# Optimization experiments

Hardware: AMD Instinct MI355X
Metric: run time of the kernel (lower is better)

Reference implementation:

```python
import jax, jax.numpy as jnp
import numpy as np

N_SRC, N_DST, E = 10000, 40000, 1_280_000
IN_DIM, OUT_DIM, FEAT, O_DIM = 128, 64, 64, 300


def setup_inputs() -> dict:
    key = jax.random.key(0)
    ks = jax.random.split(key, 10)
    s = 0.05
    return {
        "h": jax.random.normal(ks[0], (N_SRC, IN_DIM), jnp.float32),
        "o": jax.random.normal(ks[1], (N_DST, O_DIM), jnp.float32),
        "tfidf": jax.random.normal(ks[2], (E, FEAT), jnp.float32),
        "W_fc": jax.random.normal(ks[3], (IN_DIM, OUT_DIM), jnp.float32) * s,
        "W_fc1": jax.random.normal(ks[4], (O_DIM, OUT_DIM), jnp.float32) * s,
        "W_feat": jax.random.normal(ks[5], (FEAT, OUT_DIM), jnp.float32) * s,
        "b_feat": jax.random.normal(ks[6], (OUT_DIM,), jnp.float32) * s,
        "W_attn": jax.random.normal(ks[7], (OUT_DIM, 1), jnp.float32) * s,
        "edge_src": jax.random.randint(ks[8], (E,), 0, N_SRC, jnp.int32),
        "edge_dst": jax.random.randint(ks[9], (E,), 0, N_DST, jnp.int32),
    }


def reference(h, o, tfidf, W_fc, W_fc1, W_feat, b_feat, W_attn, edge_src, edge_dst):
    n_dst = o.shape[0]
    # node projections: z on sentence (src) nodes via fc, on word (dst) nodes via fc1
    z_src = h @ W_fc                      # [N_SRC, D]
    z_dst = o @ W_fc1                     # [N_DST, D]
    # edge attention: z2 = src.z + dst.z + feat_fc(tfidfembed)
    dfeat = tfidf @ W_feat + b_feat       # [E, D]
    z2 = z_src[edge_src] + z_dst[edge_dst] + dfeat
    z3 = jnp.where(z2 > 0, z2, 0.01 * z2)  # leaky_relu, torch default slope
    e = (z3 @ W_attn)[:, 0]               # [E]
    # segment softmax over incoming edges of each dst (word) node
    m = jax.ops.segment_max(e, edge_dst, num_segments=n_dst)   # [N_DST]
    e_exp = jnp.exp(e - m[edge_dst])                           # [E]
    denom = jax.ops.segment_sum(e_exp, edge_dst, num_segments=n_dst)
    alpha = e_exp / jnp.maximum(denom, 1e-9)[edge_dst]         # [E]
    # weighted sum of src z into dst mailbox
    out = jax.ops.segment_sum(alpha[:, None] * z_src[edge_src], edge_dst,
                              num_segments=n_dst)              # [N_DST, D]
    return out
```

## Files before the change

kernel.cpp:

```cpp
#include <hip/hip_runtime.h>
#include <hip/hip_bf16.h>

#define N_SRC 10000
#define N_DST 40000
#define NE    1280000
#define IN_DIM 128
#define O_DIM  300
#define D      64
#define FEAT   64
#define NB     157

typedef __bf16 bf16x8 __attribute__((ext_vector_type(8)));
typedef __bf16 bf16x4 __attribute__((ext_vector_type(4)));
typedef float  f32x4  __attribute__((ext_vector_type(4)));

__global__ __launch_bounds__(256) void k_zsrc(const float* __restrict__ h,
                                              const float* __restrict__ Wfc,
                                              float* __restrict__ z,
                                              __bf16* __restrict__ zh){
    __shared__ float w[IN_DIM * D];
    for (int i = threadIdx.x; i < IN_DIM * D; i += blockDim.x) w[i] = Wfc[i];
    __syncthreads();
    int lane = threadIdx.x & 63;
    int wid  = blockIdx.x * 4 + (threadIdx.x >> 6);
    int nw   = gridDim.x * 4;
    for (int r0 = wid * 4; r0 < N_SRC; r0 += nw * 4){
        const f32x4* p0 = (const f32x4*)(h + (size_t)(r0 + 0) * IN_DIM);
        const f32x4* p1 = (const f32x4*)(h + (size_t)(r0 + 1) * IN_DIM);
        const f32x4* p2 = (const f32x4*)(h + (size_t)(r0 + 2) * IN_DIM);
        const f32x4* p3 = (const f32x4*)(h + (size_t)(r0 + 3) * IN_DIM);
        float a0 = 0.f, a1 = 0.f, a2 = 0.f, a3 = 0.f;
        #pragma unroll 4
        for (int k4 = 0; k4 < IN_DIM / 4; ++k4){
            f32x4 v0 = p0[k4], v1 = p1[k4], v2 = p2[k4], v3 = p3[k4];
            #pragma unroll
            for (int i = 0; i < 4; ++i){
                float wv = w[(k4 * 4 + i) * D + lane];
                a0 += v0[i] * wv; a1 += v1[i] * wv;
                a2 += v2[i] * wv; a3 += v3[i] * wv;
            }
        }
        z[(size_t)(r0 + 0) * D + lane] = a0; zh[(size_t)(r0 + 0) * D + lane] = (__bf16)a0;
        z[(size_t)(r0 + 1) * D + lane] = a1; zh[(size_t)(r0 + 1) * D + lane] = (__bf16)a1;
        z[(size_t)(r0 + 2) * D + lane] = a2; zh[(size_t)(r0 + 2) * D + lane] = (__bf16)a2;
        z[(size_t)(r0 + 3) * D + lane] = a3; zh[(size_t)(r0 + 3) * D + lane] = (__bf16)a3;
    }
}

__global__ __launch_bounds__(256) void k_zdst(const float* __restrict__ o,
                                              const float* __restrict__ Wfc1,
                                              float* __restrict__ z){
    extern __shared__ float w[];
    for (int i = threadIdx.x; i < O_DIM * D; i += blockDim.x) w[i] = Wfc1[i];
    __syncthreads();
    int lane = threadIdx.x & 63;
    int wid  = blockIdx.x * 4 + (threadIdx.x >> 6);
    int nw   = gridDim.x * 4;
    for (int r0 = wid * 4; r0 < N_DST; r0 += nw * 4){
        const f32x4* p0 = (const f32x4*)(o + (size_t)(r0 + 0) * O_DIM);
        const f32x4* p1 = (const f32x4*)(o + (size_t)(r0 + 1) * O_DIM);
        const f32x4* p2 = (const f32x4*)(o + (size_t)(r0 + 2) * O_DIM);
        const f32x4* p3 = (const f32x4*)(o + (size_t)(r0 + 3) * O_DIM);
        float a0 = 0.f, a1 = 0.f, a2 = 0.f, a3 = 0.f;
        #pragma unroll 5
        for (int k4 = 0; k4 < O_DIM / 4; ++k4){
            f32x4 v0 = p0[k4], v1 = p1[k4], v2 = p2[k4], v3 = p3[k4];
            #pragma unroll
            for (int i = 0; i < 4; ++i){
                float wv = w[(k4 * 4 + i) * D + lane];
                a0 += v0[i] * wv; a1 += v1[i] * wv;
                a2 += v2[i] * wv; a3 += v3[i] * wv;
            }
        }
        z[(size_t)(r0 + 0) * D + lane] = a0;
        z[(size_t)(r0 + 1) * D + lane] = a1;
        z[(size_t)(r0 + 2) * D + lane] = a2;
        z[(size_t)(r0 + 3) * D + lane] = a3;
    }
}

__global__ __launch_bounds__(256) void k_rank(const int* __restrict__ edst,
                                              int* __restrict__ cnt,
                                              int* __restrict__ rank){
    int i = blockIdx.x * blockDim.x + threadIdx.x;
    if (i < NE) rank[i] = atomicAdd(&cnt[edst[i]], 1);
}

__device__ __forceinline__ int block_incl_scan(int c, int* wsum){
    int lane = threadIdx.x & 63, w = threadIdx.x >> 6;
    int v = c;
    #pragma unroll
    for (int off = 1; off < 64; off <<= 1){
        int u = __shfl_up(v, off);
        if (lane >= off) v += u;
    }
    if (lane == 63) wsum[w] = v;
    __syncthreads();
    int add = 0;
    for (int ww = 0; ww < w; ++ww) add += wsum[ww];
    return v + add;
}

__global__ __launch_bounds__(256) void k_scan1(const int* __restrict__ cnt,
                                               int* __restrict__ bsum){
    __shared__ int wsum[4];
    int i = blockIdx.x * 256 + threadIdx.x;
    int c = (i < N_DST) ? cnt[i] : 0;
    int lane = threadIdx.x & 63, w = threadIdx.x >> 6;
    int v = c;
    #pragma unroll
    for (int off = 1; off < 64; off <<= 1) v += __shfl_xor(v, off);
    if (lane == 0) wsum[w] = v;
    __syncthreads();
    if (threadIdx.x == 0)
        bsum[blockIdx.x] = wsum[0] + wsum[1] + wsum[2] + wsum[3];
}

__global__ __launch_bounds__(256) void k_scan2(int* __restrict__ bsum){
    __shared__ int wsum[4];
    int i = threadIdx.x;
    int c = (i < NB) ? bsum[i] : 0;
    int v = block_incl_scan(c, wsum);
    if (i < NB) bsum[i] = v - c;
}

__global__ __launch_bounds__(256) void k_scan3(const int* __restrict__ cnt,
                                               const int* __restrict__ bsum,
                                               int* __restrict__ csr){
    __shared__ int wsum[4];
    int i = blockIdx.x * 256 + threadIdx.x;
    int c = (i < N_DST) ? cnt[i] : 0;
    int v = block_incl_scan(c, wsum);
    int val = bsum[blockIdx.x] + v - c;
    if (i < N_DST) csr[i] = val;
    if (blockIdx.x == 0 && threadIdx.x == 0) csr[N_DST] = NE;
}

__global__ __launch_bounds__(256) void k_edge(
        const float* __restrict__ tfidf,
        const int*   __restrict__ esrc, const int* __restrict__ edst,
        const int*   __restrict__ rank, const int* __restrict__ csr,
        const __bf16* __restrict__ zsrch, const float* __restrict__ zdst,
        const float* __restrict__ Wfeat, const float* __restrict__ bfeat,
        const float* __restrict__ Wattn,
        float* __restrict__ escore_p, int* __restrict__ ssrc_s){
    int lane = threadIdx.x & 63;
    int lo = lane & 15, g = lane >> 4;

    bf16x8 afr[4][2];
    #pragma unroll
    for (int mt = 0; mt < 4; ++mt){
        int m = mt * 16 + lo;
        #pragma unroll
        for (int kh = 0; kh < 2; ++kh){
            #pragma unroll
            for (int j = 0; j < 8; ++j){
                int k = kh * 32 + g * 8 + j;
                afr[mt][kh][j] = (__bf16)Wfeat[k * D + m];
            }
        }
    }
    f32x4 bf4[4], wa4[4];
    #pragma unroll
    for (int mt = 0; mt < 4; ++mt){
        int db = mt * 16 + g * 4;
        bf4[mt] = *(const f32x4*)(bfeat + db);
        wa4[mt] = *(const f32x4*)(Wattn + db);
    }

    int wid = blockIdx.x * 4 + (threadIdx.x >> 6);
    int nw  = gridDim.x * 4;
    for (int tile = wid; tile < NE / 16; tile += nw){
        int e  = tile * 16 + lo;
        int ss = esrc[e];
        int sd = edst[e];
        int rk = rank[e];

        const float* trow = tfidf + (size_t)e * FEAT;
        bf16x8 bfr[2];
        #pragma unroll
        for (int kh = 0; kh < 2; ++kh){
            f32x4 fa = *(const f32x4*)(trow + kh * 32 + g * 8);
            f32x4 fb = *(const f32x4*)(trow + kh * 32 + g * 8 + 4);
            #pragma unroll
            for (int j = 0; j < 4; ++j){
                bfr[kh][j]     = (__bf16)fa[j];
                bfr[kh][4 + j] = (__bf16)fb[j];
            }
        }

        float pacc = 0.f;
        #pragma unroll
        for (int mt = 0; mt < 4; ++mt){
            f32x4 acc = {0.f, 0.f, 0.f, 0.f};
            acc = __builtin_amdgcn_mfma_f32_16x16x32_bf16(afr[mt][0], bfr[0], acc, 0, 0, 0);
            acc = __builtin_amdgcn_mfma_f32_16x16x32_bf16(afr[mt][1], bfr[1], acc, 0, 0, 0);
            int db = mt * 16 + g * 4;
            bf16x4 zs = *(const bf16x4*)(zsrch + (size_t)ss * D + db);
            f32x4  zd = *(const f32x4*)(zdst + (size_t)sd * D + db);
            #pragma unroll
            for (int r = 0; r < 4; ++r){
                float z2 = acc[r] + (float)zs[r] + zd[r] + bf4[mt][r];
                float z3 = z2 > 0.f ? z2 : 0.01f * z2;
                pacc += z3 * wa4[mt][r];
            }
        }
        pacc += __shfl_xor(pacc, 16);
        pacc += __shfl_xor(pacc, 32);
        if (lane < 16){
            int pos = csr[sd] + rk;
            escore_p[pos] = pacc;
            ssrc_s[pos]   = ss;
        }
    }
}

__global__ __launch_bounds__(256) void k_post(const int* __restrict__ csr,
                                              const int* __restrict__ ssrc,
                                              const float* __restrict__ escore_p,
                                              const float* __restrict__ zsrc,
                                              float* __restrict__ out){
    int lane = threadIdx.x & 63;
    int d    = blockIdx.x * 4 + (threadIdx.x >> 6);
    if (d >= N_DST) return;
    int beg = csr[d], end = csr[d + 1];

    float m = -3.4e38f;
    for (int j = beg + lane; j < end; j += 64)
        m = fmaxf(m, escore_p[j]);
    #pragma unroll
    for (int off = 1; off < 64; off <<= 1)
        m = fmaxf(m, __shfl_xor(m, off));

    float ssum = 0.f;
    for (int j = beg + lane; j < end; j += 64)
        ssum += __expf(escore_p[j] - m);
    #pragma unroll
    for (int off = 1; off < 64; off <<= 1)
        ssum += __shfl_xor(ssum, off);
    float inv = 1.f / fmaxf(ssum, 1e-9f);

    float acc = 0.f;
    for (int base = beg; base < end; base += 64){
        int n = end - base; if (n > 64) n = 64;
        int   sj = 0;
        float aj = 0.f;
        if (base + lane < end){
            sj = ssrc[base + lane];
            aj = __expf(escore_p[base + lane] - m) * inv;
        }
        for (int t = 0; t < n; ++t){
            int   s = __shfl(sj, t);
            float a = __shfl(aj, t);
            acc += a * zsrc[(size_t)s * D + lane];
        }
    }
    out[(size_t)d * D + lane] = acc;
}

extern "C" void kernel_launch(void* const* d_in, const int* in_sizes, int n_in,
                              void* d_out, int out_size, void* d_ws, size_t ws_size,
                              hipStream_t stream) {
    const float* h     = (const float*)d_in[0];
    const float* o     = (const float*)d_in[1];
    const float* tfidf = (const float*)d_in[2];
    const float* Wfc   = (const float*)d_in[3];
    const float* Wfc1  = (const float*)d_in[4];
    const float* Wfeat = (const float*)d_in[5];
    const float* bfeat = (const float*)d_in[6];
    const float* Wattn = (const float*)d_in[7];
    const int*   esrc  = (const int*)d_in[8];
    const int*   edst  = (const int*)d_in[9];
    float* out = (float*)d_out;

    float*  ws      = (float*)d_ws;
    float*  zsrc    = ws;
    float*  zdst    = ws + 640000;
    __bf16* zsrch   = (__bf16*)(ws + 3200000);
    float*  escorep = ws + 3520000;
    int*    ssrc    = (int*)(ws + 4800000);
    int*    rank    = (int*)(ws + 6080000);
    int*    cnt     = (int*)(ws + 7360000);
    int*    csr     = (int*)(ws + 7400000);
    int*    bsum    = (int*)(ws + 7440002);

    hipMemsetAsync(cnt, 0, N_DST * sizeof(int), stream);

    k_zsrc<<<256, 256, 0, stream>>>(h, Wfc, zsrc, zsrch);
    k_zdst<<<512, 256, O_DIM * D * sizeof(float), stream>>>(o, Wfc1, zdst);
    k_rank<<<NE / 256, 256, 0, stream>>>(edst, cnt, rank);
    k_scan1<<<NB, 256, 0, stream>>>(cnt, bsum);
    k_scan2<<<1, 256, 0, stream>>>(bsum);
    k_scan3<<<NB, 256, 0, stream>>>(cnt, bsum, csr);
    k_edge<<<4096, 256, 0, stream>>>(tfidf, esrc, edst, rank, csr, zsrch, zdst,
                                     Wfeat, bfeat, Wattn, escorep, ssrc);
    k_post<<<N_DST / 4, 256, 0, stream>>>(csr, ssrc, escorep, zsrc, out);
}
```

Measured before the change: 857.3 us.

## Software-pipeline edge index loads and unroll gather loop in post kernel

In the edge kernel, the next tile's src/dst indices and CSR position are prefetched while the current tile runs. The z_src/z_dst gathers are hoisted ahead of the MFMAs, and tfidf is read with nontemporal loads. The edge grid is halved so each wave handles more tiles and the prefetch has more to hide. The post kernel's weighted gather is unrolled by four to keep more independent loads in flight, at the cost of more registers.

Measured after the change: 806.6 us. 1.06x faster.

```diff
diff --git a/kernel.cpp b/kernel.cpp
--- a/kernel.cpp
+++ b/kernel.cpp
@@ -168,25 +168,50 @@
         wa4[mt] = *(const f32x4*)(Wattn + db);
     }
 
+    const int NT = NE / 16;
     int wid = blockIdx.x * 4 + (threadIdx.x >> 6);
     int nw  = gridDim.x * 4;
-    for (int tile = wid; tile < NE / 16; tile += nw){
-        int e  = tile * 16 + lo;
-        int ss = esrc[e];
-        int sd = edst[e];
-        int rk = rank[e];
-
-        const float* trow = tfidf + (size_t)e * FEAT;
+
+    int tile = wid;
+    int nss = 0, nsd = 0, npos = 0;
+    if (tile < NT){
+        int e = tile * 16 + lo;
+        nss = esrc[e]; nsd = edst[e];
+        npos = csr[nsd] + rank[e];
+    }
+
+    for (; tile < NT; tile += nw){
+        int css = nss, csd = nsd, cpos = npos;
+
+        bf16x4 zs[4]; f32x4 zd[4];
+        #pragma unroll
+        for (int mt = 0; mt < 4; ++mt){
+            int db = mt * 16 + g * 4;
+            zs[mt] = *(const bf16x4*)(zsrch + (size_t)css * D + db);
+            zd[mt] = *(const f32x4*)(zdst  + (size_t)csd * D + db);
+        }
+
+        int e0 = tile * 16 + lo;
+        const float* trow = tfidf + (size_t)e0 * FEAT;
+        f32x4 fa0 = __builtin_nontemporal_load((const f32x4*)(trow + g * 8));
+        f32x4 fb0 = __builtin_nontemporal_load((const f32x4*)(trow + g * 8 + 4));
+        f32x4 fa1 = __builtin_nontemporal_load((const f32x4*)(trow + 32 + g * 8));
+        f32x4 fb1 = __builtin_nontemporal_load((const f32x4*)(trow + 32 + g * 8 + 4));
+
+        int tn = tile + nw;
+        if (tn < NT){
+            int en = tn * 16 + lo;
+            nss = esrc[en]; nsd = edst[en];
+            npos = csr[nsd] + rank[en];
+        }
+
         bf16x8 bfr[2];
         #pragma unroll
-        for (int kh = 0; kh < 2; ++kh){
-            f32x4 fa = *(const f32x4*)(trow + kh * 32 + g * 8);
-            f32x4 fb = *(const f32x4*)(trow + kh * 32 + g * 8 + 4);
-            #pragma unroll
-            for (int j = 0; j < 4; ++j){
-                bfr[kh][j]     = (__bf16)fa[j];
-                bfr[kh][4 + j] = (__bf16)fb[j];
-            }
+        for (int j = 0; j < 4; ++j){
+            bfr[0][j]     = (__bf16)fa0[j];
+            bfr[0][4 + j] = (__bf16)fb0[j];
+            bfr[1][j]     = (__bf16)fa1[j];
+            bfr[1][4 + j] = (__bf16)fb1[j];
         }
 
         float pacc = 0.f;
@@ -195,12 +220,9 @@
             f32x4 acc = {0.f, 0.f, 0.f, 0.f};
             acc = __builtin_amdgcn_mfma_f32_16x16x32_bf16(afr[mt][0], bfr[0], acc, 0, 0, 0);
             acc = __builtin_amdgcn_mfma_f32_16x16x32_bf16(afr[mt][1], bfr[1], acc, 0, 0, 0);
-            int db = mt * 16 + g * 4;
-            bf16x4 zs = *(const bf16x4*)(zsrch + (size_t)ss * D + db);
-            f32x4  zd = *(const f32x4*)(zdst + (size_t)sd * D + db);
             #pragma unroll
             for (int r = 0; r < 4; ++r){
-                float z2 = acc[r] + (float)zs[r] + zd[r] + bf4[mt][r];
+                float z2 = acc[r] + (float)zs[mt][r] + zd[mt][r] + bf4[mt][r];
                 float z3 = z2 > 0.f ? z2 : 0.01f * z2;
                 pacc += z3 * wa4[mt][r];
             }
@@ -208,9 +230,8 @@
         pacc += __shfl_xor(pacc, 16);
         pacc += __shfl_xor(pacc, 32);
         if (lane < 16){
-            int pos = csr[sd] + rk;
-            escore_p[pos] = pacc;
-            ssrc_s[pos]   = ss;
+            escore_p[cpos] = pacc;
+            ssrc_s[cpos]   = css;
         }
     }
 }
@@ -249,7 +270,19 @@
             sj = ssrc[base + lane];
             aj = __expf(escore_p[base + lane] - m) * inv;
         }
-        for (int t = 0; t < n; ++t){
+        int t = 0;
+        for (; t + 4 <= n; t += 4){
+            int   s0 = __shfl(sj, t + 0), s1 = __shfl(sj, t + 1);
+            int   s2 = __shfl(sj, t + 2), s3 = __shfl(sj, t + 3);
+            float a0 = __shfl(aj, t + 0), a1 = __shfl(aj, t + 1);
+            float a2 = __shfl(aj, t + 2), a3 = __shfl(aj, t + 3);
+            float v0 = zsrc[(size_t)s0 * D + lane];
+            float v1 = zsrc[(size_t)s1 * D + lane];
+            float v2 = zsrc[(size_t)s2 * D + lane];
+            float v3 = zsrc[(size_t)s3 * D + lane];
+            acc += a0 * v0; acc += a1 * v1; acc += a2 * v2; acc += a3 * v3;
+        }
+        for (; t < n; ++t){
             int   s = __shfl(sj, t);
             float a = __shfl(aj, t);
             acc += a * zsrc[(size_t)s * D + lane];
@@ -292,7 +325,7 @@
     k_scan1<<<NB, 256, 0, stream>>>(cnt, bsum);
     k_scan2<<<1, 256, 0, stream>>>(bsum);
     k_scan3<<<NB, 256, 0, stream>>>(cnt, bsum, csr);
-    k_edge<<<4096, 256, 0, stream>>>(tfidf, esrc, edst, rank, csr, zsrch, zdst,
+    k_edge<<<2048, 256, 0, stream>>>(tfidf, esrc, edst, rank, csr, zsrch, zdst,
                                      Wfeat, bfeat, Wattn, escorep, ssrc);
     k_post<<<N_DST / 4, 256, 0, stream>>>(csr, ssrc, escorep, zsrc, out);
 }
```
